# Optimization experiments

Measured on AMD Instinct MI355X. Metric: run time of the kernel, lower is better.

Reference implementation:

```python
import jax, jax.numpy as jnp
import numpy as np

N = 50000   # nodes
E = 800000  # edges (avg degree 16)
R = 3       # relations (distance bins)
IN = 3      # node_input_dim
H = 64      # hidden_dim
EA = 6      # edge_input_dim
DH = 32     # decoder_hidden_dim


def setup_inputs() -> dict:
    key = jax.random.key(0)
    ks = jax.random.split(key, 16)
    x = jax.random.normal(ks[0], (N, IN), jnp.float32)
    edge_index = jax.random.randint(ks[1], (2, E), 0, N)
    edge_attr = jax.random.uniform(ks[2], (E, EA), dtype=jnp.float32)
    # scale log1p-distance column so edges span all 3 bins (thresholds ~8.52, ~9.21)
    edge_attr = edge_attr.at[:, 0].mul(12.0)
    p = lambda k, s: jax.random.normal(k, s, jnp.float32) * 0.1
    return dict(
        x=x, edge_index=edge_index, edge_attr=edge_attr,
        w0=p(ks[3], (R, IN, H)), root0=p(ks[4], (IN, H)), b0=jnp.zeros((H,), jnp.float32),
        w1=p(ks[5], (R, H, H)),  root1=p(ks[6], (H, H)),  b1=jnp.zeros((H,), jnp.float32),
        w2=p(ks[7], (R, H, H)),  root2=p(ks[8], (H, H)),  b2=jnp.zeros((H,), jnp.float32),
        ln_g0=jnp.ones((H,), jnp.float32), ln_b0=jnp.zeros((H,), jnp.float32),
        ln_g1=jnp.ones((H,), jnp.float32), ln_b1=jnp.zeros((H,), jnp.float32),
        ln_g2=jnp.ones((H,), jnp.float32), ln_b2=jnp.zeros((H,), jnp.float32),
        res_w=p(ks[9], (IN, H)), res_b=jnp.zeros((H,), jnp.float32),
        dec_w1=p(ks[10], (4 * H + EA, DH)), dec_b1=jnp.zeros((DH,), jnp.float32),
        dec_w2=p(ks[11], (DH, DH // 2)),    dec_b2=jnp.zeros((DH // 2,), jnp.float32),
        dec_w3=p(ks[12], (DH // 2, 1)),     dec_b3=jnp.zeros((1,), jnp.float32),
    )


def _layernorm(v, g, b, eps=1e-5):
    mu = v.mean(-1, keepdims=True)
    var = ((v - mu) ** 2).mean(-1, keepdims=True)
    return (v - mu) / jnp.sqrt(var + eps) * g + b


def reference(x, edge_index, edge_attr,
              w0, root0, b0, w1, root1, b1, w2, root2, b2,
              ln_g0, ln_b0, ln_g1, ln_b1, ln_g2, ln_b2,
              res_w, res_b,
              dec_w1, dec_b1, dec_w2, dec_b2, dec_w3, dec_b3):
    dist = edge_attr[:, 0]
    q1 = jnp.log1p(jnp.float32(5000.0))
    q2 = jnp.log1p(jnp.float32(10000.0))
    edge_type = (dist > q1).astype(jnp.int32) + (dist > q2).astype(jnp.int32)  # [E]
    src, dst = edge_index[0], edge_index[1]

    def rgcn(xi, W, root, b):
        # RGCNConv with per-relation mean aggregation:
        # out_i = root x_i + b + sum_r W_r * mean_{j in N_r(i)} x_j
        # aggregate-then-transform: segment-sum masked source feats, divide by
        # per-relation in-degree, then one small [in,H] matmul per relation.
        xs = xi[src]                                  # [E, in] gather
        out = xi @ root + b                           # [N, H]
        for r in range(R):
            m = (edge_type == r).astype(xi.dtype)[:, None]
            s = jax.ops.segment_sum(xs * m, dst, num_segments=N)   # [N, in]
            c = jax.ops.segment_sum(m, dst, num_segments=N)        # [N, 1]
            out = out + (s / jnp.maximum(c, 1.0)) @ W[r]
        return out

    # encoder (eval mode -> dropout is identity)
    h = jax.nn.relu(rgcn(x, w0, root0, b0))
    h1 = _layernorm(h + x @ res_w + res_b, ln_g0, ln_b0)
    h = jax.nn.relu(rgcn(h1, w1, root1, b1))
    h2 = _layernorm(h + h1, ln_g1, ln_b1)
    h = jax.nn.relu(rgcn(h2, w2, root2, b2))
    h3 = _layernorm(h + h2, ln_g2, ln_b2)

    # edge decoder
    hs, hd = h3[src], h3[dst]                         # [E, H] gathers
    dec_in = jnp.concatenate([hs, hd, jnp.abs(hs - hd), hs * hd, edge_attr], axis=-1)
    z = jax.nn.relu(dec_in @ dec_w1 + dec_b1)
    z = jax.nn.relu(z @ dec_w2 + dec_b2)
    return (z @ dec_w3 + dec_b3).squeeze(-1)          # [E]
```

## Files before the change

### kernel.cpp

```cpp
#include <hip/hip_runtime.h>
#include <math.h>

#define NN 50000
#define NE 800000
#define HD 64
#define NB 196

typedef float f32x4 __attribute__((ext_vector_type(4)));
typedef float f32x16 __attribute__((ext_vector_type(16)));
typedef short short8 __attribute__((ext_vector_type(8)));
typedef _Float16 hf2 __attribute__((ext_vector_type(2)));
typedef _Float16 half8 __attribute__((ext_vector_type(8)));

__device__ __forceinline__ float wave_sum(float v) {
  #pragma unroll
  for (int off = 32; off > 0; off >>= 1) v += __shfl_xor(v, off, 64);
  return v;
}

__device__ __forceinline__ unsigned f2h_pk(float a, float b) {
  auto v = __builtin_amdgcn_cvt_pkrtz(a, b);
  union { decltype(v) h; unsigned u; } cv; cv.h = v; return cv.u;
}
__device__ __forceinline__ unsigned short f2h(float a) {
  union { _Float16 h; unsigned short u; } cv; cv.h = (_Float16)a; return cv.u;
}
__device__ __forceinline__ float h2f(unsigned short b) {
  union { unsigned short u; _Float16 h; } v; v.u = b; return (float)v.h;
}

__global__ __launch_bounds__(256) void edge_prep(
    const int* __restrict__ ei, const float* __restrict__ ea,
    int* __restrict__ cntR, unsigned char* __restrict__ r8)
{
  int e = blockIdx.x * blockDim.x + threadIdx.x;
  if (e >= NE) return;
  float dist = ea[e * 6];
  const float q1 = log1pf(5000.0f);
  const float q2 = log1pf(10000.0f);
  int r = (dist > q1 ? 1 : 0) + (dist > q2 ? 1 : 0);
  r8[e] = (unsigned char)r;
  int d = ei[NE + e];
  atomicAdd(&cntR[d * 3 + r], 1);
}

__global__ __launch_bounds__(256) void scanA(const int* __restrict__ cntR, int* __restrict__ bsum) {
  __shared__ int sd[256];
  int n = blockIdx.x * 256 + threadIdx.x;
  int deg = 0;
  if (n < NN) deg = cntR[3 * n] + cntR[3 * n + 1] + cntR[3 * n + 2];
  sd[threadIdx.x] = deg;
  __syncthreads();
  #pragma unroll
  for (int s = 128; s > 0; s >>= 1) {
    if (threadIdx.x < s) sd[threadIdx.x] += sd[threadIdx.x + s];
    __syncthreads();
  }
  if (threadIdx.x == 0) bsum[blockIdx.x] = sd[0];
}

__global__ __launch_bounds__(256) void scanB(int* __restrict__ bsum) {
  __shared__ int sd[256];
  int v = (threadIdx.x < NB) ? bsum[threadIdx.x] : 0;
  sd[threadIdx.x] = v;
  __syncthreads();
  for (int s = 1; s < 256; s <<= 1) {
    int t = (threadIdx.x >= s) ? sd[threadIdx.x - s] : 0;
    __syncthreads();
    sd[threadIdx.x] += t;
    __syncthreads();
  }
  if (threadIdx.x < NB) bsum[threadIdx.x] = sd[threadIdx.x] - v;
}

__global__ __launch_bounds__(256) void scanC(
    const int* __restrict__ cntR, const int* __restrict__ bsum,
    int* __restrict__ off3, int* __restrict__ cursor3, float* __restrict__ dinv)
{
  __shared__ int sd[256];
  int n = blockIdx.x * 256 + threadIdx.x;
  int c0 = 0, c1 = 0, c2 = 0;
  if (n < NN) { c0 = cntR[3 * n]; c1 = cntR[3 * n + 1]; c2 = cntR[3 * n + 2]; }
  int deg = c0 + c1 + c2;
  sd[threadIdx.x] = deg;
  __syncthreads();
  for (int s = 1; s < 256; s <<= 1) {
    int t = (threadIdx.x >= s) ? sd[threadIdx.x - s] : 0;
    __syncthreads();
    sd[threadIdx.x] += t;
    __syncthreads();
  }
  if (n < NN) {
    int o = bsum[blockIdx.x] + sd[threadIdx.x] - deg;
    off3[3 * n + 0] = o;           cursor3[3 * n + 0] = o;
    off3[3 * n + 1] = o + c0;      cursor3[3 * n + 1] = o + c0;
    off3[3 * n + 2] = o + c0 + c1; cursor3[3 * n + 2] = o + c0 + c1;
    dinv[3 * n + 0] = 1.0f / (float)(c0 > 1 ? c0 : 1);
    dinv[3 * n + 1] = 1.0f / (float)(c1 > 1 ? c1 : 1);
    dinv[3 * n + 2] = 1.0f / (float)(c2 > 1 ? c2 : 1);
  }
}

__global__ __launch_bounds__(256) void scatter_kernel(
    const int* __restrict__ ei, const unsigned char* __restrict__ r8,
    int* __restrict__ cursor3, unsigned short* __restrict__ sorted)
{
  int e = blockIdx.x * blockDim.x + threadIdx.x;
  if (e >= NE) return;
  int r = r8[e];
  int s = ei[e], d = ei[NE + e];
  int pos = atomicAdd(&cursor3[d * 3 + r], 1);
  sorted[pos] = (unsigned short)s;
}

__global__ __launch_bounds__(256) void agg0_pack(
    const float* __restrict__ x, const int* __restrict__ off3, const int* __restrict__ cntR,
    const unsigned short* __restrict__ sorted, float* __restrict__ agg0,
    const float* __restrict__ W1, const float* __restrict__ W2,
    const float* __restrict__ root1, const float* __restrict__ w1,
    const float* __restrict__ root2, const float* __restrict__ w2,
    unsigned short* __restrict__ pk3, unsigned short* __restrict__ pk2,
    unsigned short* __restrict__ pkl1, unsigned short* __restrict__ pkl2)
{
  if (blockIdx.x < 3) {
    if (blockIdx.x == 0) {
      for (int idx = threadIdx.x; idx < 8704; idx += 256) {
        int j = idx & 7, l = (idx >> 3) & 63, t = idx >> 9;
        int k = 16 * t + 8 * (l >> 5) + j;
        int n = l & 31;
        pk3[idx] = (k < 262) ? f2h(W1[k * 32 + n]) : (unsigned short)0;
      }
      for (int idx = threadIdx.x; idx < 512; idx += 256) {
        int j = idx & 7, l = idx >> 3;
        int k = (l >> 4) * 8 + j, n = l & 15;
        pk2[idx] = f2h(W2[k * 16 + n]);
      }
    } else {
      const float* root = (blockIdx.x == 1) ? root1 : root2;
      const float* W    = (blockIdx.x == 1) ? w1 : w2;
      unsigned short* pkL = (blockIdx.x == 1) ? pkl1 : pkl2;
      for (int idx = threadIdx.x; idx < 16384; idx += 256) {
        int j = idx & 7, l = (idx >> 3) & 63, nt = (idx >> 9) & 3, t = idx >> 11;
        int k = t * 32 + (l >> 4) * 8 + j;
        int n = nt * 16 + (l & 15);
        float w = (k < 64) ? root[k * 64 + n]
                           : W[((k - 64) >> 6) * 4096 + (k & 63) * 64 + n];
        pkL[idx] = f2h(w);
      }
    }
    return;
  }
  int wid = ((blockIdx.x - 3) * blockDim.x + threadIdx.x) >> 6;
  int lane = threadIdx.x & 63;
  int n = wid * 16 + (lane >> 2);
  int f = lane & 3;
  if (n >= NN) return;
  int off = off3[3 * n];
  int c0 = cntR[3 * n], c1 = cntR[3 * n + 1], c2 = cntR[3 * n + 2];
  int c01 = c0 + c1, deg = c01 + c2;
  float a0 = 0.f, a1 = 0.f, a2 = 0.f;
  for (int i = 0; i < deg; i++) {
    int s = sorted[off + i];
    float v = (f < 3) ? x[s * 3 + f] : 0.f;
    if (i < c0) a0 += v; else if (i < c01) a1 += v; else a2 += v;
  }
  if (f < 3) {
    agg0[n * 9 + 0 + f] = a0;
    agg0[n * 9 + 3 + f] = a1;
    agg0[n * 9 + 6 + f] = a2;
  }
}

__global__ __launch_bounds__(256) void node0_kernel(
    const float* __restrict__ x, const float* __restrict__ agg0, const float* __restrict__ dinv,
    const float* __restrict__ w0, const float* __restrict__ root0, const float* __restrict__ b0,
    const float* __restrict__ res_w, const float* __restrict__ res_b,
    const float* __restrict__ g, const float* __restrict__ bb,
    unsigned short* __restrict__ hb)
{
  int wid = __builtin_amdgcn_readfirstlane((int)((blockIdx.x * blockDim.x + threadIdx.x) >> 6));
  int lane = threadIdx.x & 63;
  int n0 = wid * 8;
  if (n0 >= NN) return;
  float wr[3], ww[9], wres[3];
  #pragma unroll
  for (int i = 0; i < 3; i++) { wr[i] = root0[i * HD + lane]; wres[i] = res_w[i * HD + lane]; }
  #pragma unroll
  for (int i = 0; i < 9; i++) ww[i] = w0[i * HD + lane];
  float vb = b0[lane], vrb = res_b[lane], vg = g[lane], vbb = bb[lane];
  #pragma unroll
  for (int k = 0; k < 8; k++) {
    int nk = n0 + k;
    float xv[3];
    #pragma unroll
    for (int i = 0; i < 3; i++) xv[i] = x[nk * 3 + i];
    float v = vb;
    #pragma unroll
    for (int i = 0; i < 3; i++) v = fmaf(xv[i], wr[i], v);
    #pragma unroll
    for (int r = 0; r < 3; r++) {
      float s = 0.f;
      #pragma unroll
      for (int i = 0; i < 3; i++) s = fmaf(agg0[nk * 9 + r * 3 + i], ww[r * 3 + i], s);
      v = fmaf(dinv[nk * 3 + r], s, v);
    }
    v = fmaxf(v, 0.f);
    float res = vrb;
    #pragma unroll
    for (int i = 0; i < 3; i++) res = fmaf(xv[i], wres[i], res);
    float t = v + res;
    float mu = wave_sum(t) * 0.015625f;
    float dt = t - mu;
    float var = wave_sum(dt * dt) * 0.015625f;
    float o = dt * rsqrtf(var + 1e-5f) * vg + vbb;
    hb[(size_t)nk * HD + lane] = f2h(o);
  }
}

__global__ __launch_bounds__(256) void layer_fused(
    const unsigned short* __restrict__ hb_in, const unsigned short* __restrict__ pkL,
    const float* __restrict__ bias, const float* __restrict__ g, const float* __restrict__ bb,
    const int* __restrict__ off3, const int* __restrict__ cntR,
    const unsigned short* __restrict__ sorted, const float* __restrict__ dinv,
    unsigned short* __restrict__ hb_out)
{
  __shared__ unsigned short tile[4][16][256];
  int wv = threadIdx.x >> 6;
  int lane = threadIdx.x & 63;
  int wid = (blockIdx.x * blockDim.x + threadIdx.x) >> 6;
  int n0 = wid * 16;
  if (n0 >= NN) return;
  char* T = (char*)&tile[wv][0][0];

  {
    int m = lane >> 2;
    int q = lane & 3;
    int node = n0 + m;
    int swz = (m & 7) << 4;
    const unsigned short* hrow = hb_in + (size_t)node * HD + q * 16;
    uint4 rv0 = *(const uint4*)(hrow);
    uint4 rv1 = *(const uint4*)(hrow + 8);
    *(uint4*)(T + m * 512 + ((q * 32) ^ swz))      = rv0;
    *(uint4*)(T + m * 512 + ((q * 32 + 16) ^ swz)) = rv1;

    union U4 { uint4 u; hf2 h[4]; };
    #pragma unroll
    for (int r = 0; r < 3; r++) {
      int st = off3[node * 3 + r];
      int len = cntR[node * 3 + r];
      hf2 acc[8];
      #pragma unroll
      for (int j = 0; j < 8; j++) acc[j] = (hf2){(_Float16)0.f, (_Float16)0.f};
      int i = 0;
      for (; i + 2 <= len; i += 2) {
        int s0 = sorted[st + i], s1 = sorted[st + i + 1];
        const uint4* p0 = (const uint4*)(hb_in + (size_t)s0 * HD + q * 16);
        const uint4* p1 = (const uint4*)(hb_in + (size_t)s1 * HD + q * 16);
        U4 u0, u1, v0, v1;
        u0.u = p0[0]; u1.u = p0[1]; v0.u = p1[0]; v1.u = p1[1];
        #pragma unroll
        for (int k = 0; k < 4; k++) {
          acc[k]     += u0.h[k] + v0.h[k];
          acc[4 + k] += u1.h[k] + v1.h[k];
        }
      }
      if (i < len) {
        int s0 = sorted[st + i];
        const uint4* p0 = (const uint4*)(hb_in + (size_t)s0 * HD + q * 16);
        U4 u0, u1;
        u0.u = p0[0]; u1.u = p0[1];
        #pragma unroll
        for (int k = 0; k < 4; k++) {
          acc[k]     += u0.h[k];
          acc[4 + k] += u1.h[k];
        }
      }
      float dv = dinv[node * 3 + r];
      unsigned pk[8];
      #pragma unroll
      for (int j = 0; j < 8; j++)
        pk[j] = f2h_pk((float)acc[j][0] * dv, (float)acc[j][1] * dv);
      uint4 w0 = make_uint4(pk[0], pk[1], pk[2], pk[3]);
      uint4 w1 = make_uint4(pk[4], pk[5], pk[6], pk[7]);
      *(uint4*)(T + m * 512 + ((128 + r * 128 + q * 32) ^ swz))      = w0;
      *(uint4*)(T + m * 512 + ((128 + r * 128 + q * 32 + 16) ^ swz)) = w1;
    }
  }

  asm volatile("s_waitcnt lgkmcnt(0)" ::: "memory");
  __builtin_amdgcn_sched_barrier(0);

  int m2 = lane & 15, gq = lane >> 4;
  int swz2 = (m2 & 7) << 4;
  const half8* Bp = (const half8*)pkL;
  f32x4 acc[4];
  #pragma unroll
  for (int nt = 0; nt < 4; nt++) acc[nt] = (f32x4){0.f, 0.f, 0.f, 0.f};
  #pragma unroll
  for (int t = 0; t < 8; t++) {
    union AF { short8 s; half8 h; } af;
    af.s = *(const short8*)(T + m2 * 512 + ((gq * 16 + t * 64) ^ swz2));
    #pragma unroll
    for (int nt = 0; nt < 4; nt++)
      acc[nt] = __builtin_amdgcn_mfma_f32_16x16x32_f16(af.h, Bp[(t * 4 + nt) * 64 + lane], acc[nt], 0, 0, 0);
  }

  float bias_v[4], g_v[4], bb_v[4];
  #pragma unroll
  for (int nt = 0; nt < 4; nt++) {
    bias_v[nt] = bias[nt * 16 + m2];
    g_v[nt] = g[nt * 16 + m2];
    bb_v[nt] = bb[nt * 16 + m2];
  }
  #pragma unroll
  for (int rr = 0; rr < 4; rr++) {
    int lrow = gq * 4 + rr;
    int nodeo = n0 + lrow;
    int swzr = (lrow & 7) << 4;
    float tv[4], s = 0.f;
    #pragma unroll
    for (int nt = 0; nt < 4; nt++) {
      unsigned short rh = *(const unsigned short*)(T + lrow * 512 + (((nt * 16 + m2) * 2) ^ swzr));
      float res = h2f(rh);
      float v = fmaxf(acc[nt][rr] + bias_v[nt], 0.f) + res;
      tv[nt] = v; s += v;
    }
    #pragma unroll
    for (int o = 1; o < 16; o <<= 1) s += __shfl_xor(s, o, 64);
    float mu = s * 0.015625f;
    float s2 = 0.f;
    #pragma unroll
    for (int nt = 0; nt < 4; nt++) { float dd = tv[nt] - mu; s2 += dd * dd; }
    #pragma unroll
    for (int o = 1; o < 16; o <<= 1) s2 += __shfl_xor(s2, o, 64);
    float rstd = rsqrtf(s2 * 0.015625f + 1e-5f);
    #pragma unroll
    for (int nt = 0; nt < 4; nt++) {
      float o = (tv[nt] - mu) * rstd * g_v[nt] + bb_v[nt];
      hb_out[(size_t)nodeo * HD + nt * 16 + m2] = f2h(o);
    }
  }
}

__global__ __launch_bounds__(256) void decoder_mfma(
    const unsigned short* __restrict__ hb, const int* __restrict__ ei, const float* __restrict__ ea,
    const unsigned short* __restrict__ pk3, const unsigned short* __restrict__ pk2,
    const float* __restrict__ B1, const float* __restrict__ B2,
    const float* __restrict__ W3, const float* __restrict__ B3,
    float* __restrict__ out)
{
  __shared__ float lds[4 * 32 * 33];
  int wv = threadIdx.x >> 6;
  int lane = threadIdx.x & 63;
  int e0 = (blockIdx.x * 4 + wv) * 32;
  int r = lane & 31, u = lane >> 5;

  int s = ei[e0 + r], d = ei[NE + e0 + r];
  const unsigned short* ps = hb + (size_t)s * HD + u * 8;
  const unsigned short* pq = hb + (size_t)d * HD + u * 8;

  union u8h { short8 s8; half8 h8; hf2 h[4]; unsigned w[4]; };
  u8h hs[4], hd[4];
  #pragma unroll
  for (int t = 0; t < 4; t++) {
    hs[t].s8 = *(const short8*)(ps + t * 16);
    hd[t].s8 = *(const short8*)(pq + t * 16);
  }

  u8h ad[4], pd[4];
  #pragma unroll
  for (int t = 0; t < 4; t++) {
    #pragma unroll
    for (int k = 0; k < 4; k++) {
      union { hf2 h; unsigned u; } dd;
      dd.h = hs[t].h[k] - hd[t].h[k];
      ad[t].w[k] = dd.u & 0x7FFF7FFFu;
      pd[t].h[k] = hs[t].h[k] * hd[t].h[k];
    }
  }

  u8h aea;
  aea.w[0] = 0; aea.w[1] = 0; aea.w[2] = 0; aea.w[3] = 0;
  if (u == 0) {
    const float* er = ea + (size_t)(e0 + r) * 6;
    float2 e01 = *(const float2*)(er);
    float2 e23 = *(const float2*)(er + 2);
    float2 e45 = *(const float2*)(er + 4);
    aea.w[0] = f2h_pk(e01.x, e01.y);
    aea.w[1] = f2h_pk(e23.x, e23.y);
    aea.w[2] = f2h_pk(e45.x, e45.y);
  }

  const half8* Bp = (const half8*)pk3;
  f32x16 acc = {0.f, 0.f, 0.f, 0.f, 0.f, 0.f, 0.f, 0.f,
                0.f, 0.f, 0.f, 0.f, 0.f, 0.f, 0.f, 0.f};
  #pragma unroll
  for (int t = 0; t < 4; t++)
    acc = __builtin_amdgcn_mfma_f32_32x32x16_f16(hs[t].h8, Bp[t * 64 + lane], acc, 0, 0, 0);
  #pragma unroll
  for (int t = 0; t < 4; t++)
    acc = __builtin_amdgcn_mfma_f32_32x32x16_f16(hd[t].h8, Bp[(4 + t) * 64 + lane], acc, 0, 0, 0);
  #pragma unroll
  for (int t = 0; t < 4; t++)
    acc = __builtin_amdgcn_mfma_f32_32x32x16_f16(ad[t].h8, Bp[(8 + t) * 64 + lane], acc, 0, 0, 0);
  #pragma unroll
  for (int t = 0; t < 4; t++)
    acc = __builtin_amdgcn_mfma_f32_32x32x16_f16(pd[t].h8, Bp[(12 + t) * 64 + lane], acc, 0, 0, 0);
  acc = __builtin_amdgcn_mfma_f32_32x32x16_f16(aea.h8, Bp[16 * 64 + lane], acc, 0, 0, 0);

  float* Z = lds + wv * 1056;
  float b1v = B1[r];
  #pragma unroll
  for (int i = 0; i < 16; i++) {
    int row = (i & 3) + 8 * (i >> 2) + 4 * u;
    Z[r * 33 + row] = fmaxf(acc[i] + b1v, 0.f);
  }

  int m = lane & 15, g = lane >> 4;
  float bias2 = B2[m];
  float w3v = W3[m];
  #pragma unroll
  for (int q = 0; q < 2; q++) {
    u8h A2;
    #pragma unroll
    for (int j2 = 0; j2 < 4; j2++)
      A2.w[j2] = f2h_pk(Z[(g * 8 + 2 * j2) * 33 + q * 16 + m],
                        Z[(g * 8 + 2 * j2 + 1) * 33 + q * 16 + m]);
    f32x4 acc2 = {0.f, 0.f, 0.f, 0.f};
    acc2 = __builtin_amdgcn_mfma_f32_16x16x32_f16(A2.h8, ((const half8*)pk2)[lane], acc2, 0, 0, 0);

    float t0 = fmaxf(acc2[0] + bias2, 0.f) * w3v;
    float t1 = fmaxf(acc2[1] + bias2, 0.f) * w3v;
    float t2 = fmaxf(acc2[2] + bias2, 0.f) * w3v;
    float t3 = fmaxf(acc2[3] + bias2, 0.f) * w3v;
    #pragma unroll
    for (int off = 1; off < 16; off <<= 1) {
      t0 += __shfl_xor(t0, off, 64);
      t1 += __shfl_xor(t1, off, 64);
      t2 += __shfl_xor(t2, off, 64);
      t3 += __shfl_xor(t3, off, 64);
    }
    if (m < 4) {
      float val = (m == 0) ? t0 : (m == 1) ? t1 : (m == 2) ? t2 : t3;
      out[e0 + q * 16 + g * 4 + m] = val + B3[0];
    }
  }
}

extern "C" void kernel_launch(void* const* d_in, const int* in_sizes, int n_in,
                              void* d_out, int out_size, void* d_ws, size_t ws_size,
                              hipStream_t stream) {
  const float* x      = (const float*)d_in[0];
  const int*   ei     = (const int*)d_in[1];
  const float* ea     = (const float*)d_in[2];
  const float* w0     = (const float*)d_in[3];
  const float* root0  = (const float*)d_in[4];
  const float* b0     = (const float*)d_in[5];
  const float* w1     = (const float*)d_in[6];
  const float* root1  = (const float*)d_in[7];
  const float* b1     = (const float*)d_in[8];
  const float* w2     = (const float*)d_in[9];
  const float* root2  = (const float*)d_in[10];
  const float* b2     = (const float*)d_in[11];
  const float* ln_g0  = (const float*)d_in[12];
  const float* ln_b0  = (const float*)d_in[13];
  const float* ln_g1  = (const float*)d_in[14];
  const float* ln_b1  = (const float*)d_in[15];
  const float* ln_g2  = (const float*)d_in[16];
  const float* ln_b2  = (const float*)d_in[17];
  const float* res_w  = (const float*)d_in[18];
  const float* res_b  = (const float*)d_in[19];
  const float* dec_w1 = (const float*)d_in[20];
  const float* dec_b1 = (const float*)d_in[21];
  const float* dec_w2 = (const float*)d_in[22];
  const float* dec_b2 = (const float*)d_in[23];
  const float* dec_w3 = (const float*)d_in[24];
  const float* dec_b3 = (const float*)d_in[25];

  char* ws = (char*)d_ws;
  unsigned char* r8 = (unsigned char*)(ws + 0);
  int*   cntR    = (int*)(ws + 800000);
  float* agg0    = (float*)(ws + 1400000);
  int*   bsum    = (int*)(ws + 3200000);
  int*   off3    = (int*)(ws + 3201024);
  int*   cursor3 = (int*)(ws + 3801024);
  float* dinv    = (float*)(ws + 4401024);
  unsigned short* sorted = (unsigned short*)(ws + 5001024);
  unsigned short* pk3  = (unsigned short*)(ws + 6601024);
  unsigned short* pkw2 = (unsigned short*)(ws + 6618432);
  unsigned short* pkl1 = (unsigned short*)(ws + 6619456);
  unsigned short* pkl2 = (unsigned short*)(ws + 6652224);
  unsigned short* hb   = (unsigned short*)(ws + 6684992);
  unsigned short* hb2  = (unsigned short*)(ws + 13084992);

  hipMemsetAsync(cntR, 0, 600000, stream);

  edge_prep<<<(NE + 255) / 256, 256, 0, stream>>>(ei, ea, cntR, r8);
  scanA<<<NB, 256, 0, stream>>>(cntR, bsum);
  scanB<<<1, 256, 0, stream>>>(bsum);
  scanC<<<NB, 256, 0, stream>>>(cntR, bsum, off3, cursor3, dinv);
  scatter_kernel<<<(NE + 255) / 256, 256, 0, stream>>>(ei, r8, cursor3, sorted);
  agg0_pack<<<3 + (NN + 63) / 64, 256, 0, stream>>>(x, off3, cntR, sorted, agg0,
                                                    dec_w1, dec_w2, root1, w1, root2, w2,
                                                    pk3, pkw2, pkl1, pkl2);

  const int node0_blocks = (NN / 8 + 3) / 4;
  const int fused_blocks = (NN / 16 + 3) / 4;

  node0_kernel<<<node0_blocks, 256, 0, stream>>>(x, agg0, dinv, w0, root0, b0,
                                                 res_w, res_b, ln_g0, ln_b0, hb);

  layer_fused<<<fused_blocks, 256, 0, stream>>>(hb, pkl1, b1, ln_g1, ln_b1,
                                                off3, cntR, sorted, dinv, hb2);
  layer_fused<<<fused_blocks, 256, 0, stream>>>(hb2, pkl2, b2, ln_g2, ln_b2,
                                                off3, cntR, sorted, dinv, hb);

  decoder_mfma<<<NE / 128, 256, 0, stream>>>(hb, ei, ea, pk3, pkw2, dec_b1,
                                             dec_b2, dec_w3, dec_b3, (float*)d_out);
}
```

Measured before the change: 324.3 us.

## Software-pipeline decoder over multiple edge tiles with LDS weights, unroll gathers

The decoder now has each wave handle DT=5 consecutive 32-edge tiles. It prefetches the next tile's node-embedding gathers and edge indices while the current tile's MFMAs run, and stages the packed decoder weights in LDS once per block instead of reading them from global memory for every tile. The agg0 and layer_fused neighbour aggregations are also unrolled by 4 so more gather loads are in flight per iteration. The cost is higher register pressure and fewer blocks, which could reduce occupancy. The agg0 rewrite also changes how the per-relation segments are walked.

```diff
diff --git a/kernel.cpp b/kernel.cpp
--- a/kernel.cpp
+++ b/kernel.cpp
@@ -5,6 +5,7 @@
 #define NE 800000
 #define HD 64
 #define NB 196
+#define DT 5
 
 typedef float f32x4 __attribute__((ext_vector_type(4)));
 typedef float f32x16 __attribute__((ext_vector_type(16)));
@@ -155,19 +156,25 @@
   int n = wid * 16 + (lane >> 2);
   int f = lane & 3;
   if (n >= NN) return;
-  int off = off3[3 * n];
-  int c0 = cntR[3 * n], c1 = cntR[3 * n + 1], c2 = cntR[3 * n + 2];
-  int c01 = c0 + c1, deg = c01 + c2;
-  float a0 = 0.f, a1 = 0.f, a2 = 0.f;
-  for (int i = 0; i < deg; i++) {
-    int s = sorted[off + i];
-    float v = (f < 3) ? x[s * 3 + f] : 0.f;
-    if (i < c0) a0 += v; else if (i < c01) a1 += v; else a2 += v;
-  }
-  if (f < 3) {
-    agg0[n * 9 + 0 + f] = a0;
-    agg0[n * 9 + 3 + f] = a1;
-    agg0[n * 9 + 6 + f] = a2;
+  #pragma unroll
+  for (int r = 0; r < 3; r++) {
+    int st = off3[3 * n + r], len = cntR[3 * n + r];
+    float a = 0.f;
+    int i = 0;
+    for (; i + 4 <= len; i += 4) {
+      int s0 = sorted[st + i], s1 = sorted[st + i + 1];
+      int s2 = sorted[st + i + 2], s3 = sorted[st + i + 3];
+      float v0 = (f < 3) ? x[s0 * 3 + f] : 0.f;
+      float v1 = (f < 3) ? x[s1 * 3 + f] : 0.f;
+      float v2 = (f < 3) ? x[s2 * 3 + f] : 0.f;
+      float v3 = (f < 3) ? x[s3 * 3 + f] : 0.f;
+      a += (v0 + v1) + (v2 + v3);
+    }
+    for (; i < len; i++) {
+      int s0 = sorted[st + i];
+      a += (f < 3) ? x[s0 * 3 + f] : 0.f;
+    }
+    if (f < 3) agg0[n * 9 + r * 3 + f] = a;
   }
 }
 
@@ -252,19 +259,25 @@
       #pragma unroll
       for (int j = 0; j < 8; j++) acc[j] = (hf2){(_Float16)0.f, (_Float16)0.f};
       int i = 0;
-      for (; i + 2 <= len; i += 2) {
-        int s0 = sorted[st + i], s1 = sorted[st + i + 1];
+      for (; i + 4 <= len; i += 4) {
+        int s0 = sorted[st + i],     s1 = sorted[st + i + 1];
+        int s2 = sorted[st + i + 2], s3 = sorted[st + i + 3];
         const uint4* p0 = (const uint4*)(hb_in + (size_t)s0 * HD + q * 16);
         const uint4* p1 = (const uint4*)(hb_in + (size_t)s1 * HD + q * 16);
-        U4 u0, u1, v0, v1;
-        u0.u = p0[0]; u1.u = p0[1]; v0.u = p1[0]; v1.u = p1[1];
+        const uint4* p2 = (const uint4*)(hb_in + (size_t)s2 * HD + q * 16);
+        const uint4* p3 = (const uint4*)(hb_in + (size_t)s3 * HD + q * 16);
+        U4 a0, a1, b0, b1, c0, c1, d0, d1;
+        a0.u = p0[0]; a1.u = p0[1];
+        b0.u = p1[0]; b1.u = p1[1];
+        c0.u = p2[0]; c1.u = p2[1];
+        d0.u = p3[0]; d1.u = p3[1];
         #pragma unroll
         for (int k = 0; k < 4; k++) {
-          acc[k]     += u0.h[k] + v0.h[k];
-          acc[4 + k] += u1.h[k] + v1.h[k];
+          acc[k]     += (a0.h[k] + b0.h[k]) + (c0.h[k] + d0.h[k]);
+          acc[4 + k] += (a1.h[k] + b1.h[k]) + (c1.h[k] + d1.h[k]);
         }
       }
-      if (i < len) {
+      for (; i < len; i++) {
         int s0 = sorted[st + i];
         const uint4* p0 = (const uint4*)(hb_in + (size_t)s0 * HD + q * 16);
         U4 u0, u1;
@@ -349,101 +362,146 @@
     const float* __restrict__ W3, const float* __restrict__ B3,
     float* __restrict__ out)
 {
-  __shared__ float lds[4 * 32 * 33];
+  __shared__ float Zl[4 * 32 * 33];
+  __shared__ unsigned short Bsh[8704 + 512];
+  {
+    unsigned* dsh = (unsigned*)Bsh;
+    const unsigned* sp3 = (const unsigned*)pk3;
+    for (int i = threadIdx.x; i < 4352; i += 256) dsh[i] = sp3[i];
+    const unsigned* sp2 = (const unsigned*)pk2;
+    if (threadIdx.x < 256) dsh[4352 + threadIdx.x] = sp2[threadIdx.x];
+  }
+  __syncthreads();
+
   int wv = threadIdx.x >> 6;
   int lane = threadIdx.x & 63;
-  int e0 = (blockIdx.x * 4 + wv) * 32;
   int r = lane & 31, u = lane >> 5;
-
-  int s = ei[e0 + r], d = ei[NE + e0 + r];
-  const unsigned short* ps = hb + (size_t)s * HD + u * 8;
-  const unsigned short* pq = hb + (size_t)d * HD + u * 8;
-
-  union u8h { short8 s8; half8 h8; hf2 h[4]; unsigned w[4]; };
-  u8h hs[4], hd[4];
-  #pragma unroll
-  for (int t = 0; t < 4; t++) {
-    hs[t].s8 = *(const short8*)(ps + t * 16);
-    hd[t].s8 = *(const short8*)(pq + t * 16);
-  }
-
-  u8h ad[4], pd[4];
-  #pragma unroll
-  for (int t = 0; t < 4; t++) {
-    #pragma unroll
-    for (int k = 0; k < 4; k++) {
-      union { hf2 h; unsigned u; } dd;
-      dd.h = hs[t].h[k] - hd[t].h[k];
-      ad[t].w[k] = dd.u & 0x7FFF7FFFu;
-      pd[t].h[k] = hs[t].h[k] * hd[t].h[k];
-    }
-  }
-
-  u8h aea;
-  aea.w[0] = 0; aea.w[1] = 0; aea.w[2] = 0; aea.w[3] = 0;
-  if (u == 0) {
-    const float* er = ea + (size_t)(e0 + r) * 6;
-    float2 e01 = *(const float2*)(er);
-    float2 e23 = *(const float2*)(er + 2);
-    float2 e45 = *(const float2*)(er + 4);
-    aea.w[0] = f2h_pk(e01.x, e01.y);
-    aea.w[1] = f2h_pk(e23.x, e23.y);
-    aea.w[2] = f2h_pk(e45.x, e45.y);
-  }
-
-  const half8* Bp = (const half8*)pk3;
-  f32x16 acc = {0.f, 0.f, 0.f, 0.f, 0.f, 0.f, 0.f, 0.f,
-                0.f, 0.f, 0.f, 0.f, 0.f, 0.f, 0.f, 0.f};
-  #pragma unroll
-  for (int t = 0; t < 4; t++)
-    acc = __builtin_amdgcn_mfma_f32_32x32x16_f16(hs[t].h8, Bp[t * 64 + lane], acc, 0, 0, 0);
-  #pragma unroll
-  for (int t = 0; t < 4; t++)
-    acc = __builtin_amdgcn_mfma_f32_32x32x16_f16(hd[t].h8, Bp[(4 + t) * 64 + lane], acc, 0, 0, 0);
-  #pragma unroll
-  for (int t = 0; t < 4; t++)
-    acc = __builtin_amdgcn_mfma_f32_32x32x16_f16(ad[t].h8, Bp[(8 + t) * 64 + lane], acc, 0, 0, 0);
-  #pragma unroll
-  for (int t = 0; t < 4; t++)
-    acc = __builtin_amdgcn_mfma_f32_32x32x16_f16(pd[t].h8, Bp[(12 + t) * 64 + lane], acc, 0, 0, 0);
-  acc = __builtin_amdgcn_mfma_f32_32x32x16_f16(aea.h8, Bp[16 * 64 + lane], acc, 0, 0, 0);
-
-  float* Z = lds + wv * 1056;
+  int base = (blockIdx.x * 4 + wv) * 32 * DT;
+
+  int m = lane & 15, g = lane >> 4;
   float b1v = B1[r];
-  #pragma unroll
-  for (int i = 0; i < 16; i++) {
-    int row = (i & 3) + 8 * (i >> 2) + 4 * u;
-    Z[r * 33 + row] = fmaxf(acc[i] + b1v, 0.f);
-  }
-
-  int m = lane & 15, g = lane >> 4;
   float bias2 = B2[m];
   float w3v = W3[m];
-  #pragma unroll
-  for (int q = 0; q < 2; q++) {
-    u8h A2;
-    #pragma unroll
-    for (int j2 = 0; j2 < 4; j2++)
-      A2.w[j2] = f2h_pk(Z[(g * 8 + 2 * j2) * 33 + q * 16 + m],
-                        Z[(g * 8 + 2 * j2 + 1) * 33 + q * 16 + m]);
-    f32x4 acc2 = {0.f, 0.f, 0.f, 0.f};
-    acc2 = __builtin_amdgcn_mfma_f32_16x16x32_f16(A2.h8, ((const half8*)pk2)[lane], acc2, 0, 0, 0);
-
-    float t0 = fmaxf(acc2[0] + bias2, 0.f) * w3v;
-    float t1 = fmaxf(acc2[1] + bias2, 0.f) * w3v;
-    float t2 = fmaxf(acc2[2] + bias2, 0.f) * w3v;
-    float t3 = fmaxf(acc2[3] + bias2, 0.f) * w3v;
-    #pragma unroll
-    for (int off = 1; off < 16; off <<= 1) {
-      t0 += __shfl_xor(t0, off, 64);
-      t1 += __shfl_xor(t1, off, 64);
-      t2 += __shfl_xor(t2, off, 64);
-      t3 += __shfl_xor(t3, off, 64);
-    }
-    if (m < 4) {
-      float val = (m == 0) ? t0 : (m == 1) ? t1 : (m == 2) ? t2 : t3;
-      out[e0 + q * 16 + g * 4 + m] = val + B3[0];
-    }
+  float b3v = B3[0];
+  float* Z = Zl + wv * 1056;
+  const half8* Bp  = (const half8*)Bsh;
+  const half8* Bp2 = (const half8*)(Bsh + 8704);
+
+  union u8h { short8 s8; half8 h8; hf2 h[4]; unsigned w[4]; };
+
+  u8h hsA[4], hdA[4], hsB[4], hdB[4];
+  float2 E0[3], E1[3], E2[3];
+
+  auto GATH = [&](u8h* Hs, u8h* Hd, int s, int d) {
+    const unsigned short* ps = hb + (size_t)s * HD + u * 8;
+    const unsigned short* pq = hb + (size_t)d * HD + u * 8;
+    #pragma unroll
+    for (int t = 0; t < 4; t++) {
+      Hs[t].s8 = *(const short8*)(ps + t * 16);
+      Hd[t].s8 = *(const short8*)(pq + t * 16);
+    }
+  };
+  auto LDEA = [&](float2* E, int e0t) {
+    if (u == 0) {
+      const float* er = ea + (size_t)(e0t + r) * 6;
+      E[0] = *(const float2*)(er);
+      E[1] = *(const float2*)(er + 2);
+      E[2] = *(const float2*)(er + 4);
+    }
+  };
+  auto COMP = [&](u8h* Hs, u8h* Hd, float2* E, int e0t) {
+    u8h ad[4], pd[4];
+    #pragma unroll
+    for (int t = 0; t < 4; t++) {
+      #pragma unroll
+      for (int k = 0; k < 4; k++) {
+        union { hf2 h; unsigned u; } dd;
+        dd.h = Hs[t].h[k] - Hd[t].h[k];
+        ad[t].w[k] = dd.u & 0x7FFF7FFFu;
+        pd[t].h[k] = Hs[t].h[k] * Hd[t].h[k];
+      }
+    }
+    u8h aea;
+    aea.w[0] = 0; aea.w[1] = 0; aea.w[2] = 0; aea.w[3] = 0;
+    if (u == 0) {
+      aea.w[0] = f2h_pk(E[0].x, E[0].y);
+      aea.w[1] = f2h_pk(E[1].x, E[1].y);
+      aea.w[2] = f2h_pk(E[2].x, E[2].y);
+    }
+
+    f32x16 acc = {0.f, 0.f, 0.f, 0.f, 0.f, 0.f, 0.f, 0.f,
+                  0.f, 0.f, 0.f, 0.f, 0.f, 0.f, 0.f, 0.f};
+    #pragma unroll
+    for (int t = 0; t < 4; t++)
+      acc = __builtin_amdgcn_mfma_f32_32x32x16_f16(Hs[t].h8, Bp[t * 64 + lane], acc, 0, 0, 0);
+    #pragma unroll
+    for (int t = 0; t < 4; t++)
+      acc = __builtin_amdgcn_mfma_f32_32x32x16_f16(Hd[t].h8, Bp[(4 + t) * 64 + lane], acc, 0, 0, 0);
+    #pragma unroll
+    for (int t = 0; t < 4; t++)
+      acc = __builtin_amdgcn_mfma_f32_32x32x16_f16(ad[t].h8, Bp[(8 + t) * 64 + lane], acc, 0, 0, 0);
+    #pragma unroll
+    for (int t = 0; t < 4; t++)
+      acc = __builtin_amdgcn_mfma_f32_32x32x16_f16(pd[t].h8, Bp[(12 + t) * 64 + lane], acc, 0, 0, 0);
+    acc = __builtin_amdgcn_mfma_f32_32x32x16_f16(aea.h8, Bp[16 * 64 + lane], acc, 0, 0, 0);
+
+    #pragma unroll
+    for (int i = 0; i < 16; i++) {
+      int row = (i & 3) + 8 * (i >> 2) + 4 * u;
+      Z[r * 33 + row] = fmaxf(acc[i] + b1v, 0.f);
+    }
+
+    #pragma unroll
+    for (int q = 0; q < 2; q++) {
+      u8h A2;
+      #pragma unroll
+      for (int j2 = 0; j2 < 4; j2++)
+        A2.w[j2] = f2h_pk(Z[(g * 8 + 2 * j2) * 33 + q * 16 + m],
+                          Z[(g * 8 + 2 * j2 + 1) * 33 + q * 16 + m]);
+      f32x4 acc2 = {0.f, 0.f, 0.f, 0.f};
+      acc2 = __builtin_amdgcn_mfma_f32_16x16x32_f16(A2.h8, Bp2[lane], acc2, 0, 0, 0);
+
+      float t0 = fmaxf(acc2[0] + bias2, 0.f) * w3v;
+      float t1 = fmaxf(acc2[1] + bias2, 0.f) * w3v;
+      float t2 = fmaxf(acc2[2] + bias2, 0.f) * w3v;
+      float t3 = fmaxf(acc2[3] + bias2, 0.f) * w3v;
+      #pragma unroll
+      for (int off = 1; off < 16; off <<= 1) {
+        t0 += __shfl_xor(t0, off, 64);
+        t1 += __shfl_xor(t1, off, 64);
+        t2 += __shfl_xor(t2, off, 64);
+        t3 += __shfl_xor(t3, off, 64);
+      }
+      if (m < 4) {
+        float val = (m == 0) ? t0 : (m == 1) ? t1 : (m == 2) ? t2 : t3;
+        out[e0t + q * 16 + g * 4 + m] = val + b3v;
+      }
+    }
+  };
+
+  int s1, d1;
+  {
+    int s0 = ei[base + r], d0 = ei[NE + base + r];
+    LDEA(E0, base);
+    GATH(hsA, hdA, s0, d0);
+  }
+  s1 = ei[base + 32 + r]; d1 = ei[NE + base + 32 + r];
+  LDEA(E1, base + 32);
+
+  #pragma unroll
+  for (int t = 0; t < DT; t++) {
+    if (t + 1 < DT) GATH(hsB, hdB, s1, d1);
+    int s2 = 0, d2 = 0;
+    if (t + 2 < DT) {
+      s2 = ei[base + (t + 2) * 32 + r]; d2 = ei[NE + base + (t + 2) * 32 + r];
+      LDEA(E2, base + (t + 2) * 32);
+    }
+    COMP(hsA, hdA, E0, base + t * 32);
+    #pragma unroll
+    for (int k = 0; k < 4; k++) { hsA[k] = hsB[k]; hdA[k] = hdB[k]; }
+    E0[0] = E1[0]; E0[1] = E1[1]; E0[2] = E1[2];
+    E1[0] = E2[0]; E1[1] = E2[1]; E1[2] = E2[2];
+    s1 = s2; d1 = d2;
   }
 }
 
@@ -515,6 +573,6 @@
   layer_fused<<<fused_blocks, 256, 0, stream>>>(hb2, pkl2, b2, ln_g2, ln_b2,
                                                 off3, cntR, sorted, dinv, hb);
 
-  decoder_mfma<<<NE / 128, 256, 0, stream>>>(hb, ei, ea, pk3, pkw2, dec_b1,
-                                             dec_b2, dec_w3, dec_b3, (float*)d_out);
-}
+  decoder_mfma<<<NE / (128 * DT), 256, 0, stream>>>(hb, ei, ea, pk3, pkw2, dec_b1,
+                                                    dec_b2, dec_w3, dec_b3, (float*)d_out);
+}
```

Measured after the change: 326.1 us. No clear change (+0.6%).
